# Kernel optimization log

Measured on AMD Instinct MI355X. Metric: run time of the kernel, lower is better.

## Reference

```python
import jax, jax.numpy as jnp
import numpy as np

NEG_SLOPE = 0.2  # PyG GATConv default LeakyReLU slope
BN_EPS = 1e-5


def gat_layer(x, src, dst, W, a_src, a_dst, num_nodes):
    """PyG-style GATConv (no dropout, eval mode). Returns [N, H, C]."""
    H, C = a_src.shape
    h = (x @ W).reshape(-1, H, C)                       # [N,H,C]
    s_src = jnp.einsum('nhc,hc->nh', h, a_src)          # [N,H]
    s_dst = jnp.einsum('nhc,hc->nh', h, a_dst)          # [N,H]
    e = jax.nn.leaky_relu(s_src[src] + s_dst[dst], NEG_SLOPE)  # [E,H]
    # segment softmax over incoming edges of each dst node
    e_max = jax.ops.segment_max(e, dst, num_segments=num_nodes)  # [N,H]
    e_exp = jnp.exp(e - e_max[dst])
    denom = jax.ops.segment_sum(e_exp, dst, num_segments=num_nodes)
    alpha = e_exp / (denom[dst] + 1e-16)                # [E,H]
    msg = h[src] * alpha[:, :, None]                    # [E,H,C] (dominant intermediate)
    return jax.ops.segment_sum(msg, dst, num_segments=num_nodes)  # [N,H,C]


def setup_inputs() -> dict:
    key = jax.random.key(0)
    ks = jax.random.split(key, 12)
    N, Din, Hdim, Heads, Dout = 50000, 128, 128, 8, 128
    E = 150000
    inp = {}
    inp['x'] = jax.random.normal(ks[0], (N, Din), dtype=jnp.float32)
    inp['edge_index'] = jax.random.randint(ks[1], (2, E), 0, N, dtype=jnp.int64)
    sc1 = 1.0 / np.sqrt(Din)
    inp['W1'] = jax.random.uniform(ks[2], (Din, Heads * Hdim), minval=-sc1, maxval=sc1, dtype=jnp.float32)
    inp['a_src1'] = jax.random.normal(ks[3], (Heads, Hdim), dtype=jnp.float32) * 0.1
    inp['a_dst1'] = jax.random.normal(ks[4], (Heads, Hdim), dtype=jnp.float32) * 0.1
    inp['b1'] = jnp.zeros((Heads * Hdim,), dtype=jnp.float32)
    inp['gamma'] = jnp.ones((Heads * Hdim,), dtype=jnp.float32)
    inp['beta'] = jnp.zeros((Heads * Hdim,), dtype=jnp.float32)
    sc2 = 1.0 / np.sqrt(Heads * Hdim)
    inp['W2'] = jax.random.uniform(ks[5], (Heads * Hdim, Dout), minval=-sc2, maxval=sc2, dtype=jnp.float32)
    inp['a_src2'] = jax.random.normal(ks[6], (1, Dout), dtype=jnp.float32) * 0.1
    inp['a_dst2'] = jax.random.normal(ks[7], (1, Dout), dtype=jnp.float32) * 0.1
    inp['b2'] = jnp.zeros((Dout,), dtype=jnp.float32)
    return inp


def reference(x, W1, a_src1, a_dst1, b1, gamma, beta, W2, a_src2, a_dst2, b2, edge_index):
    N = x.shape[0]
    src, dst = edge_index[0], edge_index[1]
    # GAT layer 1: heads=8, concat=True
    h1 = gat_layer(x, src, dst, W1, a_src1, a_dst1, N)   # [N,8,128]
    h1 = h1.reshape(N, -1) + b1                          # [N,1024]
    # BatchNorm1d (training-mode batch stats, biased variance as in torch)
    mu = jnp.mean(h1, axis=0)
    var = jnp.var(h1, axis=0)
    h1 = gamma * (h1 - mu) * jax.lax.rsqrt(var + BN_EPS) + beta
    h1 = jax.nn.elu(h1)
    # GAT layer 2: heads=1, concat=False (mean == squeeze for 1 head)
    h2 = gat_layer(h1, src, dst, W2, a_src2, a_dst2, N)  # [N,1,128]
    return h2[:, 0, :] + b2
```

## Files before the change

kernel.cpp:

```cpp
#include <hip/hip_runtime.h>
#include <hip/hip_bf16.h>
#include <math.h>

#define NEG_SLOPE 0.2f
#define BN_EPS 1e-5f

typedef short bf16x8 __attribute__((ext_vector_type(8)));
typedef float f32x4 __attribute__((ext_vector_type(4)));

__device__ __forceinline__ float bf2f(unsigned short u) {
  union { unsigned int i; float f; } v;
  v.i = ((unsigned int)u) << 16;
  return v.f;
}
__device__ __forceinline__ unsigned short f2bf(float f) {
  union { unsigned int i; float f; } v;
  v.f = f;
  unsigned int i = v.i;
  unsigned int r = (i + 0x7fffu + ((i >> 16) & 1u)) >> 16;
  return (unsigned short)r;
}

__global__ __launch_bounds__(256) void detect_kernel(
    const unsigned int* __restrict__ xw, const unsigned int* __restrict__ eiw,
    int E, int* __restrict__ flags) {
  __shared__ int cnt[2];
  if (threadIdx.x < 2) cnt[threadIdx.x] = 0;
  __syncthreads();
  int t = threadIdx.x;
  int inrange = 0;
  for (int i = t; i < 2048; i += 256) {
    unsigned int e = (xw[i] >> 7) & 0xFFu;
    inrange += (e >= 100u && e <= 135u) ? 1 : 0;
  }
  atomicAdd(&cnt[0], inrange);
  int M = min(1024, E / 2);
  int zeros = 0;
  for (int i = t; i < M; i += 256) zeros += (eiw[2 * i + 1] == 0u) ? 1 : 0;
  atomicAdd(&cnt[1], zeros);
  __syncthreads();
  if (t == 0) {
    flags[0] = (cnt[0] > 1536) ? 1 : 0;
    flags[1] = (cnt[1] > M / 2) ? 1 : 0;
  }
}

__global__ __launch_bounds__(256) void canon_x8(
    const void* __restrict__ src, unsigned short* __restrict__ dst, int n_real,
    int n_total, const int* __restrict__ flags) {
  int i = (blockIdx.x * 256 + threadIdx.x) * 8;
  if (i >= n_total) return;
  union { bf16x8 v; unsigned short u[8]; } o;
  if (i < n_real) {
    if (flags[0]) {
      o.v = *(const bf16x8*)((const unsigned short*)src + i);
    } else {
      const float4* f = (const float4*)((const float*)src + i);
      float4 f0 = f[0];
      float4 f1 = f[1];
      o.u[0] = f2bf(f0.x); o.u[1] = f2bf(f0.y);
      o.u[2] = f2bf(f0.z); o.u[3] = f2bf(f0.w);
      o.u[4] = f2bf(f1.x); o.u[5] = f2bf(f1.y);
      o.u[6] = f2bf(f1.z); o.u[7] = f2bf(f1.w);
    }
  } else {
#pragma unroll
    for (int j = 0; j < 8; ++j) o.u[j] = 0;
  }
  *(bf16x8*)(dst + i) = o.v;
}

__global__ __launch_bounds__(256) void canon_w_t(
    const void* __restrict__ src, unsigned short* __restrict__ dst, int Kdim,
    int Ndim, const int* __restrict__ flags) {
  int i = blockIdx.x * 256 + threadIdx.x;
  if (i >= Kdim * Ndim) return;
  int k = i / Ndim, n = i - k * Ndim;
  unsigned short v = flags[0] ? ((const unsigned short*)src)[i]
                              : f2bf(((const float*)src)[i]);
  dst[(size_t)n * Kdim + k] = v;
}

__global__ __launch_bounds__(1024) void canon_params(
    const void* s0, const void* s1, const void* s2, const void* s3,
    const void* s4, const void* s5, const void* s6, const void* s7,
    unsigned short* d0, unsigned short* d1, unsigned short* d2,
    unsigned short* d3, unsigned short* d4, unsigned short* d5,
    unsigned short* d6, unsigned short* d7, const int* __restrict__ flags) {
  int b = blockIdx.x, t = threadIdx.x;
  const void* s;
  unsigned short* d;
  int n;
  switch (b) {
    case 0: s = s0; d = d0; n = 1024; break;
    case 1: s = s1; d = d1; n = 1024; break;
    case 2: s = s2; d = d2; n = 1024; break;
    case 3: s = s3; d = d3; n = 1024; break;
    case 4: s = s4; d = d4; n = 1024; break;
    case 5: s = s5; d = d5; n = 128; break;
    case 6: s = s6; d = d6; n = 128; break;
    default: s = s7; d = d7; n = 128; break;
  }
  if (t < n)
    d[t] = flags[0] ? ((const unsigned short*)s)[t]
                    : f2bf(((const float*)s)[t]);
}

__global__ __launch_bounds__(256) void canon_idx(
    const int* __restrict__ ei, int* __restrict__ eis, int* __restrict__ eid,
    int E, const int* __restrict__ flags) {
  int e = blockIdx.x * 256 + threadIdx.x;
  if (e >= E) return;
  if (flags[1]) {
    eis[e] = ei[2 * (size_t)e];
    eid[e] = ei[2 * (size_t)E + 2 * (size_t)e];
  } else {
    eis[e] = ei[e];
    eid[e] = ei[E + e];
  }
}

__global__ __launch_bounds__(256) void gemm1_fused(
    const unsigned short* __restrict__ A,
    const unsigned short* __restrict__ Bt,
    unsigned short* __restrict__ C,
    const unsigned short* __restrict__ aScr,
    const unsigned short* __restrict__ aDcr,
    float* __restrict__ ssrc,
    float* __restrict__ sdst,
    int MP) {
  __shared__ unsigned short As[64 * 128];
  __shared__ unsigned short Bs[128 * 128];
  __shared__ float wscS[4][16];
  __shared__ float wscD[4][16];

  const int tid = threadIdx.x;
  const int wid = tid >> 6;
  const int lane = tid & 63;
  const int q = lane >> 4;
  const int r = lane & 15;
  const int wm = wid * 16;
  const int m0 = blockIdx.x * 64;

  const int arow = tid >> 4;
  const int ag = tid & 15;

  bf16x8 ra[4], rb[8];
#pragma unroll
  for (int j = 0; j < 4; ++j)
    ra[j] = *(const bf16x8*)(A + (size_t)(m0 + j * 16 + arow) * 128 + ag * 8);
#pragma unroll
  for (int j = 0; j < 8; ++j)
    rb[j] = *(const bf16x8*)(Bt + (size_t)(j * 16 + arow) * 128 + ag * 8);
#pragma unroll
  for (int j = 0; j < 4; ++j) {
    int row = j * 16 + arow;
    int gs = ag ^ (row & 15);
    *(bf16x8*)(As + row * 128 + gs * 8) = ra[j];
  }
#pragma unroll
  for (int j = 0; j < 8; ++j) {
    int row = j * 16 + arow;
    int gs = ag ^ (row & 15);
    *(bf16x8*)(Bs + row * 128 + gs * 8) = rb[j];
  }
  __syncthreads();

  for (int p = 0; p < 8; ++p) {
    if (p < 7) {
#pragma unroll
      for (int j = 0; j < 8; ++j)
        rb[j] = *(const bf16x8*)(Bt +
                 (size_t)((p + 1) * 128 + j * 16 + arow) * 128 + ag * 8);
    }
    f32x4 acc[8] = {};
#pragma unroll
    for (int ks = 0; ks < 4; ++ks) {
      bf16x8 af = *(const bf16x8*)(As + (wm + r) * 128 +
                                   (((ks * 4 + q) ^ r) << 3));
#pragma unroll
      for (int ni = 0; ni < 8; ++ni) {
        bf16x8 bf = *(const bf16x8*)(Bs + (ni * 16 + r) * 128 +
                                     (((ks * 4 + q) ^ r) << 3));
        acc[ni] = __builtin_amdgcn_mfma_f32_16x16x32_bf16(af, bf, acc[ni],
                                                          0, 0, 0);
      }
    }
#pragma unroll
    for (int ni = 0; ni < 8; ++ni)
#pragma unroll
      for (int i = 0; i < 4; ++i)
        C[(size_t)(m0 + wm + q * 4 + i) * 1024 + p * 128 + ni * 16 + r] =
            f2bf(acc[ni][i]);
    float aSv[8], aDv[8];
#pragma unroll
    for (int ni = 0; ni < 8; ++ni) {
      aSv[ni] = bf2f(aScr[p * 128 + ni * 16 + r]);
      aDv[ni] = bf2f(aDcr[p * 128 + ni * 16 + r]);
    }
#pragma unroll
    for (int i = 0; i < 4; ++i) {
      float ps = 0.f, pd = 0.f;
#pragma unroll
      for (int ni = 0; ni < 8; ++ni) {
        ps += acc[ni][i] * aSv[ni];
        pd += acc[ni][i] * aDv[ni];
      }
      ps += __shfl_xor(ps, 1, 64); pd += __shfl_xor(pd, 1, 64);
      ps += __shfl_xor(ps, 2, 64); pd += __shfl_xor(pd, 2, 64);
      ps += __shfl_xor(ps, 4, 64); pd += __shfl_xor(pd, 4, 64);
      ps += __shfl_xor(ps, 8, 64); pd += __shfl_xor(pd, 8, 64);
      if (r == 0) {
        wscS[wid][q * 4 + i] = ps;
        wscD[wid][q * 4 + i] = pd;
      }
    }
    if (lane < 16)
      ssrc[(size_t)p * MP + m0 + wm + lane] = wscS[wid][lane];
    else if (lane < 32)
      sdst[(size_t)p * MP + m0 + wm + (lane & 15)] = wscD[wid][lane & 15];
    __syncthreads();
    if (p < 7) {
#pragma unroll
      for (int j = 0; j < 8; ++j) {
        int row = j * 16 + arow;
        int gs = ag ^ (row & 15);
        *(bf16x8*)(Bs + row * 128 + gs * 8) = rb[j];
      }
      __syncthreads();
    }
  }
}

__global__ __launch_bounds__(256) void gemm2_bn(
    const unsigned short* __restrict__ A,
    const unsigned short* __restrict__ Bt,
    float* __restrict__ C,
    const float* __restrict__ scale, const float* __restrict__ shift,
    const unsigned short* __restrict__ aScr,
    const unsigned short* __restrict__ aDcr,
    float* __restrict__ ssrc, float* __restrict__ sdst) {
  constexpr int K = 1024;
  constexpr int BK = 64;
  constexpr int LDA = BK + 8;
  __shared__ unsigned short As[64 * LDA];
  __shared__ unsigned short Bs[128 * LDA];
  __shared__ float sS[2][64];
  __shared__ float sD[2][64];

  const int m0 = blockIdx.x * 64;
  const int tid = threadIdx.x;
  const int wid = tid >> 6;
  const int lane = tid & 63;
  const int q = lane >> 4;
  const int r = lane & 15;
  const int wm = (wid >> 1) * 32;
  const int wn = (wid & 1) * 64;

  f32x4 acc[2][4] = {};

  const int row0 = tid >> 3;
  const int col0 = (tid & 7) * 8;

  bf16x8 ra[2], rb[4];
#pragma unroll
  for (int ca = 0; ca < 2; ++ca)
    ra[ca] = *(const bf16x8*)(A + (size_t)(m0 + row0 + ca * 32) * K + col0);
#pragma unroll
  for (int cb = 0; cb < 4; ++cb)
    rb[cb] = *(const bf16x8*)(Bt + (size_t)(row0 + cb * 32) * K + col0);

  for (int k0 = 0; k0 < K; k0 += BK) {
    float scv[8], shv[8];
    *(float4*)&scv[0] = *(const float4*)(scale + k0 + col0);
    *(float4*)&scv[4] = *(const float4*)(scale + k0 + col0 + 4);
    *(float4*)&shv[0] = *(const float4*)(shift + k0 + col0);
    *(float4*)&shv[4] = *(const float4*)(shift + k0 + col0 + 4);
#pragma unroll
    for (int ca = 0; ca < 2; ++ca) {
      union { bf16x8 v; unsigned short u[8]; } pk;
      pk.v = ra[ca];
#pragma unroll
      for (int j = 0; j < 8; ++j) {
        float f = bf2f(pk.u[j]) * scv[j] + shv[j];
        f = f > 0.f ? f : (__expf(f) - 1.0f);
        pk.u[j] = f2bf(f);
      }
      *(bf16x8*)(&As[(row0 + ca * 32) * LDA + col0]) = pk.v;
    }
#pragma unroll
    for (int cb = 0; cb < 4; ++cb)
      *(bf16x8*)(&Bs[(row0 + cb * 32) * LDA + col0]) = rb[cb];
    __syncthreads();

    int k1 = k0 + BK;
    if (k1 < K) {
#pragma unroll
      for (int ca = 0; ca < 2; ++ca)
        ra[ca] = *(const bf16x8*)(A + (size_t)(m0 + row0 + ca * 32) * K + k1 +
                                  col0);
#pragma unroll
      for (int cb = 0; cb < 4; ++cb)
        rb[cb] = *(const bf16x8*)(Bt + (size_t)(row0 + cb * 32) * K + k1 +
                                  col0);
    }

#pragma unroll
    for (int ks = 0; ks < BK; ks += 32) {
      bf16x8 af[2], bfv[4];
#pragma unroll
      for (int mi = 0; mi < 2; ++mi)
        af[mi] = *(const bf16x8*)(&As[(wm + mi * 16 + r) * LDA + ks + q * 8]);
#pragma unroll
      for (int ni = 0; ni < 4; ++ni)
        bfv[ni] = *(const bf16x8*)(&Bs[(wn + ni * 16 + r) * LDA + ks + q * 8]);
#pragma unroll
      for (int mi = 0; mi < 2; ++mi)
#pragma unroll
        for (int ni = 0; ni < 4; ++ni)
          acc[mi][ni] = __builtin_amdgcn_mfma_f32_16x16x32_bf16(
              af[mi], bfv[ni], acc[mi][ni], 0, 0, 0);
    }
    __syncthreads();
  }

#pragma unroll
  for (int mi = 0; mi < 2; ++mi)
#pragma unroll
    for (int ni = 0; ni < 4; ++ni)
#pragma unroll
      for (int i = 0; i < 4; ++i) {
        int row = m0 + wm + mi * 16 + q * 4 + i;
        int col = wn + ni * 16 + r;
        C[(size_t)row * 128 + col] = acc[mi][ni][i];
      }

  const int half = wid & 1;
  float aSv[4], aDv[4];
#pragma unroll
  for (int ni = 0; ni < 4; ++ni) {
    aSv[ni] = bf2f(aScr[wn + ni * 16 + r]);
    aDv[ni] = bf2f(aDcr[wn + ni * 16 + r]);
  }
#pragma unroll
  for (int mi = 0; mi < 2; ++mi) {
#pragma unroll
    for (int i = 0; i < 4; ++i) {
      float ps = 0.f, pd = 0.f;
#pragma unroll
      for (int ni = 0; ni < 4; ++ni) {
        float v = acc[mi][ni][i];
        ps += v * aSv[ni];
        pd += v * aDv[ni];
      }
      ps += __shfl_xor(ps, 1, 64); pd += __shfl_xor(pd, 1, 64);
      ps += __shfl_xor(ps, 2, 64); pd += __shfl_xor(pd, 2, 64);
      ps += __shfl_xor(ps, 4, 64); pd += __shfl_xor(pd, 4, 64);
      ps += __shfl_xor(ps, 8, 64); pd += __shfl_xor(pd, 8, 64);
      if (r == 0) {
        int rl = wm + mi * 16 + q * 4 + i;
        sS[half][rl] = ps;
        sD[half][rl] = pd;
      }
    }
  }
  __syncthreads();
  if (tid < 64) {
    ssrc[m0 + tid] = sS[0][tid] + sS[1][tid];
    sdst[m0 + tid] = sD[0][tid] + sD[1][tid];
  }
}

__global__ __launch_bounds__(256) void count_dst(const int* __restrict__ eid,
                                                 int E, int* __restrict__ cnt) {
  int e = blockIdx.x * 256 + threadIdx.x;
  if (e < E) atomicAdd(&cnt[eid[e]], 1);
}

__global__ __launch_bounds__(256) void scan_p1(const int* __restrict__ cnt,
                                               int* __restrict__ bsum, int N) {
  __shared__ int sd[256];
  int b = blockIdx.x, t = threadIdx.x;
  int base = b * 2048;
  int s = 0;
  for (int i = t; i < 2048; i += 256) {
    int idx = base + i;
    if (idx < N) s += cnt[idx];
  }
  sd[t] = s;
  __syncthreads();
  for (int o = 128; o > 0; o >>= 1) {
    if (t < o) sd[t] += sd[t + o];
    __syncthreads();
  }
  if (t == 0) bsum[b] = sd[0];
}

__global__ __launch_bounds__(256) void scan_p2(int* __restrict__ bsum, int nb) {
  __shared__ int sd[256];
  int t = threadIdx.x;
  int own = (t < nb) ? bsum[t] : 0;
  sd[t] = own;
  __syncthreads();
  for (int o = 1; o < 256; o <<= 1) {
    int v = (t >= o) ? sd[t - o] : 0;
    __syncthreads();
    sd[t] += v;
    __syncthreads();
  }
  if (t < nb) bsum[t] = sd[t] - own;
}

__global__ __launch_bounds__(256) void scan_p3(
    const int* __restrict__ cnt, const int* __restrict__ bsum,
    int* __restrict__ offsets, int* __restrict__ cursor, int N) {
  __shared__ int sd[256];
  int b = blockIdx.x, t = threadIdx.x;
  int base = b * 2048 + t * 8;
  int c[8];
  int ts = 0;
#pragma unroll
  for (int j = 0; j < 8; ++j) {
    int idx = base + j;
    c[j] = (idx < N) ? cnt[idx] : 0;
    ts += c[j];
  }
  sd[t] = ts;
  __syncthreads();
  for (int o = 1; o < 256; o <<= 1) {
    int v = (t >= o) ? sd[t - o] : 0;
    __syncthreads();
    sd[t] += v;
    __syncthreads();
  }
  int run = bsum[b] + sd[t] - ts;
#pragma unroll
  for (int j = 0; j < 8; ++j) {
    int idx = base + j;
    if (idx < N) {
      offsets[idx] = run;
      cursor[idx] = run;
      run += c[j];
    }
  }
  if (b == gridDim.x - 1 && t == 255) offsets[N] = bsum[b] + sd[255];
}

__global__ __launch_bounds__(256) void scatter_src(
    const int* __restrict__ eis, const int* __restrict__ eid, int E,
    int* __restrict__ cursor, int* __restrict__ srcs) {
  int e = blockIdx.x * 256 + threadIdx.x;
  if (e >= E) return;
  int d = eid[e];
  int pos = atomicAdd(&cursor[d], 1);
  srcs[pos] = eis[e];
}

__global__ __launch_bounds__(256) void agg1_csr(
    const int* __restrict__ offsets, const int* __restrict__ srcs,
    const unsigned short* __restrict__ h1, const float* __restrict__ ssrc,
    const float* __restrict__ sdst, const unsigned short* __restrict__ b1,
    unsigned short* __restrict__ h1n, int N, int MP) {
  int n = blockIdx.x * 4 + (threadIdx.x >> 6);
  if (n >= N) return;
  int lane = threadIdx.x & 63;
  int c0 = lane * 8;
  int c1 = 512 + c0;
  int hA = lane >> 4;
  const float* sSA = ssrc + (size_t)hA * MP;
  const float* sSB = ssrc + (size_t)(hA + 4) * MP;
  int beg = offsets[n], end = offsets[n + 1];
  float sdA = sdst[(size_t)hA * MP + n];
  float sdB = sdst[(size_t)(hA + 4) * MP + n];
  float accA[8] = {}, accB[8] = {};
  float wsA = 0.f, wsB = 0.f;
  int p = beg;
  for (; p + 2 <= end; p += 2) {
    int s0 = srcs[p], s1 = srcs[p + 1];
    float vA0 = sSA[s0] + sdA;
    float vB0 = sSB[s0] + sdB;
    float vA1 = sSA[s1] + sdA;
    float vB1 = sSB[s1] + sdB;
    union { bf16x8 v; unsigned short u[8]; } uA0, uB0, uA1, uB1;
    uA0.v = *(const bf16x8*)(h1 + (size_t)s0 * 1024 + c0);
    uB0.v = *(const bf16x8*)(h1 + (size_t)s0 * 1024 + c1);
    uA1.v = *(const bf16x8*)(h1 + (size_t)s1 * 1024 + c0);
    uB1.v = *(const bf16x8*)(h1 + (size_t)s1 * 1024 + c1);
    vA0 = vA0 > 0.f ? vA0 : NEG_SLOPE * vA0;
    vB0 = vB0 > 0.f ? vB0 : NEG_SLOPE * vB0;
    vA1 = vA1 > 0.f ? vA1 : NEG_SLOPE * vA1;
    vB1 = vB1 > 0.f ? vB1 : NEG_SLOPE * vB1;
    float wA0 = __expf(vA0), wB0 = __expf(vB0);
    float wA1 = __expf(vA1), wB1 = __expf(vB1);
    wsA += wA0 + wA1;
    wsB += wB0 + wB1;
#pragma unroll
    for (int j = 0; j < 8; ++j) {
      accA[j] = fmaf(bf2f(uA0.u[j]), wA0, accA[j]);
      accB[j] = fmaf(bf2f(uB0.u[j]), wB0, accB[j]);
      accA[j] = fmaf(bf2f(uA1.u[j]), wA1, accA[j]);
      accB[j] = fmaf(bf2f(uB1.u[j]), wB1, accB[j]);
    }
  }
  if (p < end) {
    int s0 = srcs[p];
    float vA0 = sSA[s0] + sdA;
    float vB0 = sSB[s0] + sdB;
    union { bf16x8 v; unsigned short u[8]; } uA0, uB0;
    uA0.v = *(const bf16x8*)(h1 + (size_t)s0 * 1024 + c0);
    uB0.v = *(const bf16x8*)(h1 + (size_t)s0 * 1024 + c1);
    vA0 = vA0 > 0.f ? vA0 : NEG_SLOPE * vA0;
    vB0 = vB0 > 0.f ? vB0 : NEG_SLOPE * vB0;
    float wA0 = __expf(vA0), wB0 = __expf(vB0);
    wsA += wA0;
    wsB += wB0;
#pragma unroll
    for (int j = 0; j < 8; ++j) {
      accA[j] = fmaf(bf2f(uA0.u[j]), wA0, accA[j]);
      accB[j] = fmaf(bf2f(uB0.u[j]), wB0, accB[j]);
    }
  }
  float invA = 1.0f / (wsA + 1e-16f);
  float invB = 1.0f / (wsB + 1e-16f);
  union { bf16x8 v; unsigned short u[8]; } bA, bB, oA, oB;
  bA.v = *(const bf16x8*)(b1 + c0);
  bB.v = *(const bf16x8*)(b1 + c1);
#pragma unroll
  for (int j = 0; j < 8; ++j) {
    oA.u[j] = f2bf(accA[j] * invA + bf2f(bA.u[j]));
    oB.u[j] = f2bf(accB[j] * invB + bf2f(bB.u[j]));
  }
  *(bf16x8*)(h1n + (size_t)n * 1024 + c0) = oA.v;
  *(bf16x8*)(h1n + (size_t)n * 1024 + c1) = oB.v;
}

__global__ __launch_bounds__(256) void bn_stats_part(
    const unsigned short* __restrict__ h1n, float* __restrict__ part, int N,
    int rowsPerBlock) {
  int b = blockIdx.x;
  int half = threadIdx.x >> 7;
  int t = threadIdx.x & 127;
  int c = t * 8;
  int r0 = b * rowsPerBlock;
  int r1 = min(r0 + rowsPerBlock, N);
  float s[8] = {0, 0, 0, 0, 0, 0, 0, 0};
  float q[8] = {0, 0, 0, 0, 0, 0, 0, 0};
  int r = r0 + half;
  for (; r + 2 < r1; r += 4) {
    union { bf16x8 v; unsigned short u[8]; } u0, u1;
    u0.v = *(const bf16x8*)(h1n + (size_t)r * 1024 + c);
    u1.v = *(const bf16x8*)(h1n + (size_t)(r + 2) * 1024 + c);
#pragma unroll
    for (int j = 0; j < 8; ++j) {
      float v0 = bf2f(u0.u[j]);
      float v1 = bf2f(u1.u[j]);
      s[j] += v0 + v1;
      q[j] = fmaf(v0, v0, q[j]);
      q[j] = fmaf(v1, v1, q[j]);
    }
  }
  for (; r < r1; r += 2) {
    union { bf16x8 v; unsigned short u[8]; } u0;
    u0.v = *(const bf16x8*)(h1n + (size_t)r * 1024 + c);
#pragma unroll
    for (int j = 0; j < 8; ++j) {
      float v0 = bf2f(u0.u[j]);
      s[j] += v0;
      q[j] = fmaf(v0, v0, q[j]);
    }
  }
  float* pb = part + ((size_t)b * 2 + half) * 2048;
#pragma unroll
  for (int j = 0; j < 8; ++j) {
    pb[c + j] = s[j];
    pb[1024 + c + j] = q[j];
  }
}

__global__ __launch_bounds__(256) void bn_reduce_finalize(
    const float* __restrict__ part, int nparts,
    const unsigned short* __restrict__ gamma,
    const unsigned short* __restrict__ beta, float* __restrict__ scale,
    float* __restrict__ shift, int N) {
  int c = blockIdx.x * 4 + (threadIdx.x >> 6);
  int lane = threadIdx.x & 63;
  float s = 0.f, q = 0.f;
  for (int b = lane; b < nparts; b += 64) {
    s += part[(size_t)b * 2048 + c];
    q += part[(size_t)b * 2048 + 1024 + c];
  }
#pragma unroll
  for (int o = 32; o > 0; o >>= 1) {
    s += __shfl_xor(s, o, 64);
    q += __shfl_xor(q, o, 64);
  }
  if (lane == 0) {
    float inv_n = 1.0f / (float)N;
    float mu = s * inv_n;
    float var = q * inv_n - mu * mu;
    float sc = bf2f(gamma[c]) * rsqrtf(var + BN_EPS);
    scale[c] = sc;
    shift[c] = bf2f(beta[c]) - mu * sc;
  }
}

__global__ __launch_bounds__(256) void agg2_csr(
    const int* __restrict__ offsets, const int* __restrict__ srcs,
    const float* __restrict__ h2, const float* __restrict__ ssrc,
    const float* __restrict__ sdst, const unsigned short* __restrict__ b2,
    void* __restrict__ out, const int* __restrict__ flags, int N) {
  int n = blockIdx.x * 8 + (threadIdx.x >> 5);
  if (n >= N) return;
  int c = (threadIdx.x & 31) * 4;
  int beg = offsets[n], end = offsets[n + 1];
  float sd = sdst[n];
  float a0 = 0.f, a1 = 0.f, a2 = 0.f, a3 = 0.f, wsum = 0.f;
  int p = beg;
  for (; p + 2 <= end; p += 2) {
    int s0 = srcs[p], s1 = srcs[p + 1];
    float v0 = ssrc[s0] + sd;
    float v1 = ssrc[s1] + sd;
    float4 u0 = *(const float4*)(h2 + (size_t)s0 * 128 + c);
    float4 u1 = *(const float4*)(h2 + (size_t)s1 * 128 + c);
    v0 = v0 > 0.f ? v0 : NEG_SLOPE * v0;
    v1 = v1 > 0.f ? v1 : NEG_SLOPE * v1;
    float w0 = __expf(v0), w1 = __expf(v1);
    wsum += w0 + w1;
    a0 = fmaf(u0.x, w0, a0);
    a1 = fmaf(u0.y, w0, a1);
    a2 = fmaf(u0.z, w0, a2);
    a3 = fmaf(u0.w, w0, a3);
    a0 = fmaf(u1.x, w1, a0);
    a1 = fmaf(u1.y, w1, a1);
    a2 = fmaf(u1.z, w1, a2);
    a3 = fmaf(u1.w, w1, a3);
  }
  if (p < end) {
    int s0 = srcs[p];
    float v0 = ssrc[s0] + sd;
    float4 u0 = *(const float4*)(h2 + (size_t)s0 * 128 + c);
    v0 = v0 > 0.f ? v0 : NEG_SLOPE * v0;
    float w0 = __expf(v0);
    wsum += w0;
    a0 = fmaf(u0.x, w0, a0);
    a1 = fmaf(u0.y, w0, a1);
    a2 = fmaf(u0.z, w0, a2);
    a3 = fmaf(u0.w, w0, a3);
  }
  float inv = 1.0f / (wsum + 1e-16f);
  ushort4 bb = *(const ushort4*)(b2 + c);
  float r0 = a0 * inv + bf2f(bb.x);
  float r1 = a1 * inv + bf2f(bb.y);
  float r2 = a2 * inv + bf2f(bb.z);
  float r3 = a3 * inv + bf2f(bb.w);
  if (flags[0]) {
    ushort4 o;
    o.x = f2bf(r0); o.y = f2bf(r1); o.z = f2bf(r2); o.w = f2bf(r3);
    *(ushort4*)((unsigned short*)out + (size_t)n * 128 + c) = o;
  } else {
    *(float4*)((float*)out + (size_t)n * 128 + c) =
        make_float4(r0, r1, r2, r3);
  }
}

extern "C" void kernel_launch(void* const* d_in, const int* in_sizes, int n_in,
                              void* d_out, int out_size, void* d_ws,
                              size_t ws_size, hipStream_t stream) {
  const void* x      = d_in[0];
  const int*  ei     = (const int*)d_in[1];
  const void* W1     = d_in[2];
  const void* a_src1 = d_in[3];
  const void* a_dst1 = d_in[4];
  const void* b1     = d_in[5];
  const void* gamma  = d_in[6];
  const void* beta   = d_in[7];
  const void* W2     = d_in[8];
  const void* a_src2 = d_in[9];
  const void* a_dst2 = d_in[10];
  const void* b2     = d_in[11];

  const int N = in_sizes[0] / 128;
  const int E = in_sizes[1] / 2;
  const int MP = ((N + 127) / 128) * 128;
  const int NB = (N + 2047) / 2048;
  const int NSTAT = 256;
  const int RPB = (N + NSTAT - 1) / NSTAT;

  char* ws = (char*)d_ws;
  size_t off = 0;
  unsigned short* h1  = (unsigned short*)(ws + off); off += (size_t)MP * 1024 * 2;
  char* h1n_base = ws + off;
  unsigned short* h1n = (unsigned short*)h1n_base;   off += (size_t)MP * 1024 * 2;
  float* ssrc1 = (float*)(ws + off); off += (size_t)MP * 8 * 4;
  float* sdst1 = (float*)(ws + off); off += (size_t)MP * 8 * 4;
  int* offsets = (int*)(ws + off); off += ((size_t)(N + 1) * 4 + 63) & ~63ull;
  int* srcs    = (int*)(ws + off); off += (size_t)E * 4;
  float* part  = (float*)(ws + off); off += (size_t)NSTAT * 2 * 2048 * 4;
  unsigned short* W1t = (unsigned short*)(ws + off); off += 131072 * 2;
  unsigned short* W2t = (unsigned short*)(ws + off); off += 131072 * 2;
  unsigned short* as1c = (unsigned short*)(ws + off); off += 1024 * 2;
  unsigned short* ad1c = (unsigned short*)(ws + off); off += 1024 * 2;
  unsigned short* b1c  = (unsigned short*)(ws + off); off += 1024 * 2;
  unsigned short* gmc  = (unsigned short*)(ws + off); off += 1024 * 2;
  unsigned short* btc  = (unsigned short*)(ws + off); off += 1024 * 2;
  unsigned short* as2c = (unsigned short*)(ws + off); off += 128 * 2;
  unsigned short* ad2c = (unsigned short*)(ws + off); off += 128 * 2;
  unsigned short* b2c  = (unsigned short*)(ws + off); off += 128 * 2;
  float* scale = (float*)(ws + off); off += 1024 * 4;
  float* shift = (float*)(ws + off); off += 1024 * 4;
  int* bsum    = (int*)(ws + off); off += 256 * 4;
  int* flags   = (int*)(ws + off); off += 64;
  unsigned short* x_bf = (unsigned short*)h1n_base;
  int* eis    = (int*)(h1n_base + (16u << 20));
  int* eid    = eis + E;
  int* cnt    = eid + E;
  int* cursor = cnt + N;
  float* h2    = (float*)h1;
  float* ssrc2 = ssrc1;
  float* sdst2 = sdst1;

  detect_kernel<<<1, 256, 0, stream>>>((const unsigned int*)x,
                                       (const unsigned int*)ei, E, flags);
  canon_x8<<<(MP * 128 / 8 + 255) / 256, 256, 0, stream>>>(x, x_bf, N * 128,
                                                           MP * 128, flags);
  canon_w_t<<<(131072 + 255) / 256, 256, 0, stream>>>(W1, W1t, 128, 1024, flags);
  canon_w_t<<<(131072 + 255) / 256, 256, 0, stream>>>(W2, W2t, 1024, 128, flags);
  canon_params<<<8, 1024, 0, stream>>>(a_src1, a_dst1, b1, gamma, beta, a_src2,
                                       a_dst2, b2, as1c, ad1c, b1c, gmc, btc,
                                       as2c, ad2c, b2c, flags);
  canon_idx<<<(E + 255) / 256, 256, 0, stream>>>(ei, eis, eid, E, flags);

  hipMemsetAsync(cnt, 0, (size_t)N * 4, stream);
  hipMemsetAsync((char*)h1n + (size_t)N * 1024 * 2, 0,
                 (size_t)(MP - N) * 1024 * 2, stream);

  count_dst<<<(E + 255) / 256, 256, 0, stream>>>(eid, E, cnt);
  scan_p1<<<NB, 256, 0, stream>>>(cnt, bsum, N);
  scan_p2<<<1, 256, 0, stream>>>(bsum, NB);
  scan_p3<<<NB, 256, 0, stream>>>(cnt, bsum, offsets, cursor, N);
  scatter_src<<<(E + 255) / 256, 256, 0, stream>>>(eis, eid, E, cursor, srcs);

  gemm1_fused<<<MP / 64, 256, 0, stream>>>(x_bf, W1t, h1, as1c, ad1c, ssrc1,
                                           sdst1, MP);
  agg1_csr<<<(N + 3) / 4, 256, 0, stream>>>(offsets, srcs, h1, ssrc1, sdst1,
                                            b1c, h1n, N, MP);

  bn_stats_part<<<NSTAT, 256, 0, stream>>>(h1n, part, N, RPB);
  bn_reduce_finalize<<<256, 256, 0, stream>>>(part, NSTAT * 2, gmc, btc, scale,
                                              shift, N);

  gemm2_bn<<<MP / 64, 256, 0, stream>>>(h1n, W2t, h2, scale, shift, as2c,
                                        ad2c, ssrc2, sdst2);
  agg2_csr<<<(N + 7) / 8, 256, 0, stream>>>(offsets, srcs, h2, ssrc2, sdst2,
                                            b2c, d_out, flags, N);
}
```

Measured before the change: 358.8 us.

## Fuse BN statistics into layer-1 aggregation and switch scores to node-major layout

Layer-1 aggregation becomes a persistent grid-stride kernel that also accumulates per-channel sum and sum-of-squares of its bf16 output, reduces them across waves in shared memory, and atomically adds them into 256 partial buffers. This removes the separate bn_stats_part pass that re-read all of h1n. The attention scores from gemm1 are now stored node-major ([N][8]) with one coalesced float4 store per block, so each gather reads neighbouring heads from the same cache line. In exchange it adds a memset for the partial buffers, float atomics whose order makes the sums nondeterministic, and fixes the aggregation grid at 2048 blocks.

Result: slower. 366.7 us (+2.2%).

```diff
diff --git a/kernel.cpp b/kernel.cpp
--- a/kernel.cpp
+++ b/kernel.cpp
@@ -131,8 +131,8 @@
     int MP) {
   __shared__ unsigned short As[64 * 128];
   __shared__ unsigned short Bs[128 * 128];
-  __shared__ float wscS[4][16];
-  __shared__ float wscD[4][16];
+  __shared__ float sAll[64][8];
+  __shared__ float dAll[64][8];
 
   const int tid = threadIdx.x;
   const int wid = tid >> 6;
@@ -211,14 +211,10 @@
       ps += __shfl_xor(ps, 4, 64); pd += __shfl_xor(pd, 4, 64);
       ps += __shfl_xor(ps, 8, 64); pd += __shfl_xor(pd, 8, 64);
       if (r == 0) {
-        wscS[wid][q * 4 + i] = ps;
-        wscD[wid][q * 4 + i] = pd;
-      }
-    }
-    if (lane < 16)
-      ssrc[(size_t)p * MP + m0 + wm + lane] = wscS[wid][lane];
-    else if (lane < 32)
-      sdst[(size_t)p * MP + m0 + wm + (lane & 15)] = wscD[wid][lane & 15];
+        sAll[wm + q * 4 + i][p] = ps;
+        dAll[wm + q * 4 + i][p] = pd;
+      }
+    }
     __syncthreads();
     if (p < 7) {
 #pragma unroll
@@ -229,6 +225,14 @@
       }
       __syncthreads();
     }
+  }
+  __syncthreads();
+  if (tid < 128) {
+    float4 v = *((const float4*)&sAll[0][0] + tid);
+    *((float4*)(ssrc + (size_t)m0 * 8) + tid) = v;
+  } else {
+    float4 v = *((const float4*)&dAll[0][0] + (tid - 128));
+    *((float4*)(sdst + (size_t)m0 * 8) + (tid - 128)) = v;
   }
 }
 
@@ -460,120 +464,107 @@
     const int* __restrict__ offsets, const int* __restrict__ srcs,
     const unsigned short* __restrict__ h1, const float* __restrict__ ssrc,
     const float* __restrict__ sdst, const unsigned short* __restrict__ b1,
-    unsigned short* __restrict__ h1n, int N, int MP) {
-  int n = blockIdx.x * 4 + (threadIdx.x >> 6);
-  if (n >= N) return;
-  int lane = threadIdx.x & 63;
-  int c0 = lane * 8;
-  int c1 = 512 + c0;
-  int hA = lane >> 4;
-  const float* sSA = ssrc + (size_t)hA * MP;
-  const float* sSB = ssrc + (size_t)(hA + 4) * MP;
-  int beg = offsets[n], end = offsets[n + 1];
-  float sdA = sdst[(size_t)hA * MP + n];
-  float sdB = sdst[(size_t)(hA + 4) * MP + n];
-  float accA[8] = {}, accB[8] = {};
-  float wsA = 0.f, wsB = 0.f;
-  int p = beg;
-  for (; p + 2 <= end; p += 2) {
-    int s0 = srcs[p], s1 = srcs[p + 1];
-    float vA0 = sSA[s0] + sdA;
-    float vB0 = sSB[s0] + sdB;
-    float vA1 = sSA[s1] + sdA;
-    float vB1 = sSB[s1] + sdB;
-    union { bf16x8 v; unsigned short u[8]; } uA0, uB0, uA1, uB1;
-    uA0.v = *(const bf16x8*)(h1 + (size_t)s0 * 1024 + c0);
-    uB0.v = *(const bf16x8*)(h1 + (size_t)s0 * 1024 + c1);
-    uA1.v = *(const bf16x8*)(h1 + (size_t)s1 * 1024 + c0);
-    uB1.v = *(const bf16x8*)(h1 + (size_t)s1 * 1024 + c1);
-    vA0 = vA0 > 0.f ? vA0 : NEG_SLOPE * vA0;
-    vB0 = vB0 > 0.f ? vB0 : NEG_SLOPE * vB0;
-    vA1 = vA1 > 0.f ? vA1 : NEG_SLOPE * vA1;
-    vB1 = vB1 > 0.f ? vB1 : NEG_SLOPE * vB1;
-    float wA0 = __expf(vA0), wB0 = __expf(vB0);
-    float wA1 = __expf(vA1), wB1 = __expf(vB1);
-    wsA += wA0 + wA1;
-    wsB += wB0 + wB1;
-#pragma unroll
-    for (int j = 0; j < 8; ++j) {
-      accA[j] = fmaf(bf2f(uA0.u[j]), wA0, accA[j]);
-      accB[j] = fmaf(bf2f(uB0.u[j]), wB0, accB[j]);
-      accA[j] = fmaf(bf2f(uA1.u[j]), wA1, accA[j]);
-      accB[j] = fmaf(bf2f(uB1.u[j]), wB1, accB[j]);
-    }
-  }
-  if (p < end) {
-    int s0 = srcs[p];
-    float vA0 = sSA[s0] + sdA;
-    float vB0 = sSB[s0] + sdB;
-    union { bf16x8 v; unsigned short u[8]; } uA0, uB0;
-    uA0.v = *(const bf16x8*)(h1 + (size_t)s0 * 1024 + c0);
-    uB0.v = *(const bf16x8*)(h1 + (size_t)s0 * 1024 + c1);
-    vA0 = vA0 > 0.f ? vA0 : NEG_SLOPE * vA0;
-    vB0 = vB0 > 0.f ? vB0 : NEG_SLOPE * vB0;
-    float wA0 = __expf(vA0), wB0 = __expf(vB0);
-    wsA += wA0;
-    wsB += wB0;
-#pragma unroll
-    for (int j = 0; j < 8; ++j) {
-      accA[j] = fmaf(bf2f(uA0.u[j]), wA0, accA[j]);
-      accB[j] = fmaf(bf2f(uB0.u[j]), wB0, accB[j]);
-    }
-  }
-  float invA = 1.0f / (wsA + 1e-16f);
-  float invB = 1.0f / (wsB + 1e-16f);
-  union { bf16x8 v; unsigned short u[8]; } bA, bB, oA, oB;
+    unsigned short* __restrict__ h1n, float* __restrict__ part, int N) {
+  __shared__ float redS[4][1024];
+  __shared__ float redQ[4][1024];
+  const int tid = threadIdx.x;
+  const int wid = tid >> 6;
+  const int lane = tid & 63;
+  const int c0 = lane * 8;
+  const int c1 = 512 + c0;
+  const int hA = lane >> 4;
+  union { bf16x8 v; unsigned short u[8]; } bA, bB;
   bA.v = *(const bf16x8*)(b1 + c0);
   bB.v = *(const bf16x8*)(b1 + c1);
+  float bs0[8] = {}, bs1[8] = {}, bq0[8] = {}, bq1[8] = {};
+  const int stride = gridDim.x * 4;
+  for (int n = blockIdx.x * 4 + wid; n < N; n += stride) {
+    int beg = offsets[n], end = offsets[n + 1];
+    float sdA = sdst[n * 8 + hA];
+    float sdB = sdst[n * 8 + hA + 4];
+    float accA[8] = {}, accB[8] = {};
+    float wsA = 0.f, wsB = 0.f;
+    int p = beg;
+    for (; p + 2 <= end; p += 2) {
+      int s0 = srcs[p], s1 = srcs[p + 1];
+      float vA0 = ssrc[s0 * 8 + hA] + sdA;
+      float vB0 = ssrc[s0 * 8 + hA + 4] + sdB;
+      float vA1 = ssrc[s1 * 8 + hA] + sdA;
+      float vB1 = ssrc[s1 * 8 + hA + 4] + sdB;
+      union { bf16x8 v; unsigned short u[8]; } uA0, uB0, uA1, uB1;
+      uA0.v = *(const bf16x8*)(h1 + (size_t)s0 * 1024 + c0);
+      uB0.v = *(const bf16x8*)(h1 + (size_t)s0 * 1024 + c1);
+      uA1.v = *(const bf16x8*)(h1 + (size_t)s1 * 1024 + c0);
+      uB1.v = *(const bf16x8*)(h1 + (size_t)s1 * 1024 + c1);
+      vA0 = vA0 > 0.f ? vA0 : NEG_SLOPE * vA0;
+      vB0 = vB0 > 0.f ? vB0 : NEG_SLOPE * vB0;
+      vA1 = vA1 > 0.f ? vA1 : NEG_SLOPE * vA1;
+      vB1 = vB1 > 0.f ? vB1 : NEG_SLOPE * vB1;
+      float wA0 = __expf(vA0), wB0 = __expf(vB0);
+      float wA1 = __expf(vA1), wB1 = __expf(vB1);
+      wsA += wA0 + wA1;
+      wsB += wB0 + wB1;
+#pragma unroll
+      for (int j = 0; j < 8; ++j) {
+        accA[j] = fmaf(bf2f(uA0.u[j]), wA0, accA[j]);
+        accB[j] = fmaf(bf2f(uB0.u[j]), wB0, accB[j]);
+        accA[j] = fmaf(bf2f(uA1.u[j]), wA1, accA[j]);
+        accB[j] = fmaf(bf2f(uB1.u[j]), wB1, accB[j]);
+      }
+    }
+    if (p < end) {
+      int s0 = srcs[p];
+      float vA0 = ssrc[s0 * 8 + hA] + sdA;
+      float vB0 = ssrc[s0 * 8 + hA + 4] + sdB;
+      union { bf16x8 v; unsigned short u[8]; } uA0, uB0;
+      uA0.v = *(const bf16x8*)(h1 + (size_t)s0 * 1024 + c0);
+      uB0.v = *(const bf16x8*)(h1 + (size_t)s0 * 1024 + c1);
+      vA0 = vA0 > 0.f ? vA0 : NEG_SLOPE * vA0;
+      vB0 = vB0 > 0.f ? vB0 : NEG_SLOPE * vB0;
+      float wA0 = __expf(vA0), wB0 = __expf(vB0);
+      wsA += wA0;
+      wsB += wB0;
+#pragma unroll
+      for (int j = 0; j < 8; ++j) {
+        accA[j] = fmaf(bf2f(uA0.u[j]), wA0, accA[j]);
+        accB[j] = fmaf(bf2f(uB0.u[j]), wB0, accB[j]);
+      }
+    }
+    float invA = 1.0f / (wsA + 1e-16f);
+    float invB = 1.0f / (wsB + 1e-16f);
+    union { bf16x8 v; unsigned short u[8]; } oA, oB;
+#pragma unroll
+    for (int j = 0; j < 8; ++j) {
+      oA.u[j] = f2bf(accA[j] * invA + bf2f(bA.u[j]));
+      oB.u[j] = f2bf(accB[j] * invB + bf2f(bB.u[j]));
+      float vA = bf2f(oA.u[j]);
+      float vB = bf2f(oB.u[j]);
+      bs0[j] += vA;
+      bq0[j] = fmaf(vA, vA, bq0[j]);
+      bs1[j] += vB;
+      bq1[j] = fmaf(vB, vB, bq1[j]);
+    }
+    *(bf16x8*)(h1n + (size_t)n * 1024 + c0) = oA.v;
+    *(bf16x8*)(h1n + (size_t)n * 1024 + c1) = oB.v;
+  }
 #pragma unroll
   for (int j = 0; j < 8; ++j) {
-    oA.u[j] = f2bf(accA[j] * invA + bf2f(bA.u[j]));
-    oB.u[j] = f2bf(accB[j] * invB + bf2f(bB.u[j]));
-  }
-  *(bf16x8*)(h1n + (size_t)n * 1024 + c0) = oA.v;
-  *(bf16x8*)(h1n + (size_t)n * 1024 + c1) = oB.v;
-}
-
-__global__ __launch_bounds__(256) void bn_stats_part(
-    const unsigned short* __restrict__ h1n, float* __restrict__ part, int N,
-    int rowsPerBlock) {
-  int b = blockIdx.x;
-  int half = threadIdx.x >> 7;
-  int t = threadIdx.x & 127;
-  int c = t * 8;
-  int r0 = b * rowsPerBlock;
-  int r1 = min(r0 + rowsPerBlock, N);
-  float s[8] = {0, 0, 0, 0, 0, 0, 0, 0};
-  float q[8] = {0, 0, 0, 0, 0, 0, 0, 0};
-  int r = r0 + half;
-  for (; r + 2 < r1; r += 4) {
-    union { bf16x8 v; unsigned short u[8]; } u0, u1;
-    u0.v = *(const bf16x8*)(h1n + (size_t)r * 1024 + c);
-    u1.v = *(const bf16x8*)(h1n + (size_t)(r + 2) * 1024 + c);
-#pragma unroll
-    for (int j = 0; j < 8; ++j) {
-      float v0 = bf2f(u0.u[j]);
-      float v1 = bf2f(u1.u[j]);
-      s[j] += v0 + v1;
-      q[j] = fmaf(v0, v0, q[j]);
-      q[j] = fmaf(v1, v1, q[j]);
-    }
-  }
-  for (; r < r1; r += 2) {
-    union { bf16x8 v; unsigned short u[8]; } u0;
-    u0.v = *(const bf16x8*)(h1n + (size_t)r * 1024 + c);
-#pragma unroll
-    for (int j = 0; j < 8; ++j) {
-      float v0 = bf2f(u0.u[j]);
-      s[j] += v0;
-      q[j] = fmaf(v0, v0, q[j]);
-    }
-  }
-  float* pb = part + ((size_t)b * 2 + half) * 2048;
-#pragma unroll
-  for (int j = 0; j < 8; ++j) {
-    pb[c + j] = s[j];
-    pb[1024 + c + j] = q[j];
+    redS[wid][c0 + j] = bs0[j];
+    redS[wid][c1 + j] = bs1[j];
+    redQ[wid][c0 + j] = bq0[j];
+    redQ[wid][c1 + j] = bq1[j];
+  }
+  __syncthreads();
+  int ch = tid * 4;
+  float* ps = part + (size_t)(blockIdx.x & 255) * 2048;
+#pragma unroll
+  for (int j = 0; j < 4; ++j) {
+    float s = redS[0][ch + j] + redS[1][ch + j] + redS[2][ch + j] +
+              redS[3][ch + j];
+    float q = redQ[0][ch + j] + redQ[1][ch + j] + redQ[2][ch + j] +
+              redQ[3][ch + j];
+    atomicAdd(ps + ch + j, s);
+    atomicAdd(ps + 1024 + ch + j, q);
   }
 }
 
@@ -683,8 +674,6 @@
   const int E = in_sizes[1] / 2;
   const int MP = ((N + 127) / 128) * 128;
   const int NB = (N + 2047) / 2048;
-  const int NSTAT = 256;
-  const int RPB = (N + NSTAT - 1) / NSTAT;
 
   char* ws = (char*)d_ws;
   size_t off = 0;
@@ -695,7 +684,7 @@
   float* sdst1 = (float*)(ws + off); off += (size_t)MP * 8 * 4;
   int* offsets = (int*)(ws + off); off += ((size_t)(N + 1) * 4 + 63) & ~63ull;
   int* srcs    = (int*)(ws + off); off += (size_t)E * 4;
-  float* part  = (float*)(ws + off); off += (size_t)NSTAT * 2 * 2048 * 4;
+  float* part  = (float*)(ws + off); off += (size_t)256 * 2048 * 4;
   unsigned short* W1t = (unsigned short*)(ws + off); off += 131072 * 2;
   unsigned short* W2t = (unsigned short*)(ws + off); off += 131072 * 2;
   unsigned short* as1c = (unsigned short*)(ws + off); off += 1024 * 2;
@@ -731,6 +720,7 @@
   canon_idx<<<(E + 255) / 256, 256, 0, stream>>>(ei, eis, eid, E, flags);
 
   hipMemsetAsync(cnt, 0, (size_t)N * 4, stream);
+  hipMemsetAsync(part, 0, (size_t)256 * 2048 * 4, stream);
   hipMemsetAsync((char*)h1n + (size_t)N * 1024 * 2, 0,
                  (size_t)(MP - N) * 1024 * 2, stream);
 
@@ -742,11 +732,9 @@
 
   gemm1_fused<<<MP / 64, 256, 0, stream>>>(x_bf, W1t, h1, as1c, ad1c, ssrc1,
                                            sdst1, MP);
-  agg1_csr<<<(N + 3) / 4, 256, 0, stream>>>(offsets, srcs, h1, ssrc1, sdst1,
-                                            b1c, h1n, N, MP);
-
-  bn_stats_part<<<NSTAT, 256, 0, stream>>>(h1n, part, N, RPB);
-  bn_reduce_finalize<<<256, 256, 0, stream>>>(part, NSTAT * 2, gmc, btc, scale,
+  agg1_csr<<<2048, 256, 0, stream>>>(offsets, srcs, h1, ssrc1, sdst1, b1c,
+                                     h1n, part, N);
+  bn_reduce_finalize<<<256, 256, 0, stream>>>(part, 256, gmc, btc, scale,
                                               shift, N);
 
   gemm2_bn<<<MP / 64, 256, 0, stream>>>(h1n, W2t, h2, scale, shift, as2c,
```
